# Kernel optimization log

Hardware: AMD Instinct MI355X
Metric: run time of the kernel (lower is better)

The kernel has to match this reference:

```python
import jax, jax.numpy as jnp
import numpy as np

A, NA, D_OBS, B = 16, 8, 64, 128  # agents, actions, obs dim, graphs
DZ = D_OBS + NA  # obs_z_input_dim = 72


def _mlp(x, W1, b1, W2, b2):
    # Linear -> leaky_relu(0.01) -> Linear, torch Linear convention (y = x @ W.T + b)
    return jax.nn.leaky_relu(x @ W1.T + b1) @ W2.T + b2


def setup_inputs() -> dict:
    key = jax.random.key(0)
    ks = iter(jax.random.split(key, 40))
    p = {}
    p["obs"] = jax.random.normal(next(ks), (B * A, D_OBS), jnp.float32)
    p["policies"] = jax.random.uniform(next(ks), (B * A, NA), jnp.float32)
    p["actions"] = jax.random.uniform(next(ks), (B * A, NA), jnp.float32)

    def mk(name, inp, out):
        p[name + "_w"] = jax.random.normal(next(ks), (out, inp), jnp.float32) / np.sqrt(inp).astype(np.float32)
        p[name + "_b"] = jax.random.normal(next(ks), (out,), jnp.float32) * 0.01

    mk("kw1", D_OBS, 64); mk("kw2", 64, 64)   # key_weight layers
    mk("qw1", D_OBS, 64); mk("qw2", 64, 64)   # query_weight layers
    mk("ko1", DZ, 64);    mk("ko2", 64, 64)   # key_obsz layers
    mk("qo1", DZ, 64);    mk("qo2", 64, 64)   # query_obsz layers
    mk("av1", DZ, 64);    mk("av2", 64, 64)   # attention_value_obsz layers
    mk("fv1", 128, 64);   mk("fv2", 64, 8)    # final_value layers
    return p


def reference(obs, policies, actions,
              kw1_w, kw1_b, kw2_w, kw2_b, qw1_w, qw1_b, qw2_w, qw2_b,
              ko1_w, ko1_b, ko2_w, ko2_b, qo1_w, qo1_b, qo2_w, qo2_b,
              av1_w, av1_b, av2_w, av2_b, fv1_w, fv1_b, fv2_w, fv2_b):
    d_k_w = jnp.sqrt(jnp.float32(kw2_w.shape[0]))
    d_k_o = jnp.sqrt(jnp.float32(ko2_w.shape[0]))
    Bn = obs.shape[0] // A
    obs_b = obs.reshape(Bn, A, -1)                      # [B,A,Dobs]
    pi = policies.reshape(Bn, A, NA)
    act = actions.reshape(Bn, A, NA)

    # --- DGL update_all on the fully-connected (with self-loop) per-batch graph ---
    key_z = _mlp(obs_b, kw1_w, kw1_b, kw2_w, kw2_b)     # [B,A,dk]
    query_z = _mlp(obs_b, qw1_w, qw1_b, qw2_w, qw2_b)
    score = jnp.einsum('bjd,bid->bij', key_z, query_z)  # src key j -> dst query i
    w = jax.nn.sigmoid(score / d_k_w)[..., None]        # [B,A,A,1], mailbox gate
    z = w * act[:, None] + (1.0 - w) * pi[:, None]      # [B,A(i),A(j),NA]
    weight_z = w.reshape(Bn * A, A, 1)

    # obs_z[b,i,j] = cat(obs[b,j], z[b,i,j])
    obs_rep = jnp.broadcast_to(obs_b[:, None], (Bn, A, A, obs_b.shape[-1]))
    obs_z = jnp.concatenate([obs_rep, z], axis=-1)      # [B,A,A,DZ]

    diag = jnp.arange(A)
    src = obs_z[:, diag, diag]                          # source_obs_z_: [B,A,DZ] (j==i entry)

    key_o = _mlp(src, ko1_w, ko1_b, ko2_w, ko2_b)       # broadcast over j
    query_o = _mlp(obs_z, qo1_w, qo1_b, qo2_w, qo2_b)   # [B,A,A,dk]
    score_o = jnp.einsum('bid,bijd->bij', key_o, query_o)
    weights_o = jax.nn.softmax(jnp.exp(jnp.clip(score_o / d_k_o, -5.0, 5.0)), axis=-1)  # [B,A,A]

    # obs_z_pi[b,i,j,k] = op[b,j] if k==j else obs_z[b,i,k], op = cat(obs, pi)
    op = jnp.concatenate([obs_b, pi], axis=-1)          # [B,A,DZ]
    m = jnp.eye(A, dtype=obs.dtype)[None, None, :, :, None]          # (j,k) mask
    obs_z_pi = obs_z[:, :, None] * (1.0 - m) + op[:, None, None] * m  # [B,A,A,A,DZ]

    attn_src = _mlp(src, av1_w, av1_b, av2_w, av2_b)                  # [B,A,O]
    attn_other = _mlp(obs_z_pi, av1_w, av1_b, av2_w, av2_b)           # [B,A,A,A,O]

    w_exp = weights_o[:, None, :, :, None]              # [b,i,j,k,1] = weights_o[b,j,k]
    mixed = jnp.mean(attn_other * w_exp, axis=-2)       # mean over k -> [B,A,A,O]
    src_rep = jnp.broadcast_to(attn_src[:, None], mixed.shape)
    node_features = jnp.concatenate([src_rep, mixed], axis=-1)        # [B,A,A,2O]
    value = _mlp(node_features, fv1_w, fv1_b, fv2_w, fv2_b)           # [B,A,A,8]

    weights_obsz = jnp.broadcast_to(w_exp, (Bn, A, A, A, 1))
    return value, weight_z, weights_obsz
```

## Files before the change

### kernel.cpp

```cpp
#include <hip/hip_runtime.h>

#define A_ 16
#define NA_ 8
#define DOBS_ 64

typedef _Float16 f16;
typedef f16 h2 __attribute__((ext_vector_type(2)));
typedef f16 v8h __attribute__((ext_vector_type(8)));
typedef float v4f __attribute__((ext_vector_type(4)));

__device__ __forceinline__ float fdot2f(h2 a, h2 b, float c) {
  return __builtin_amdgcn_fdot2(a, b, c, false);
}
__device__ __forceinline__ float lrelu(float x) { return x > 0.f ? x : 0.01f * x; }

struct P {
  const float *obs, *pol, *act;
  const float *kw1w, *kw1b, *kw2w, *kw2b, *qw1w, *qw1b, *qw2w, *qw2b;
  const float *ko1w, *ko1b, *ko2w, *ko2b, *qo1w, *qo1b, *qo2w, *qo2b;
  const float *av1w, *av1b, *av2w, *av2b, *fv1w, *fv1b, *fv2w, *fv2b;
  float *out0, *out1, *out2;
};

struct alignas(16) SM {
  f16 obsh[16 * 72];
  float pi[128];
  float act[128];
  float wsig[256];
  float wo[256];
  float c0[16];
  f16 eh[256];
  union {
    struct {
      f16 obsl[16 * 72];
      f16 Wp1[64 * 72], Wp2[64 * 72];
      f16 Wxh[64 * 72], Wxl[64 * 72];
      f16 X1h[16 * 72], X1l[16 * 72];
      f16 X2h[16 * 72], X2l[16 * 72];
      float S2[16 * 68];
      float S3G[16 * 68];
      float wz[512];
    } f;
    struct {
      f16 AOsrcD[16 * 72];
      f16 APT[64 * 24];
      f16 AextH[16 * 40];
      f16 fv2pw[512];
      f16 slice[8][1536];
      union { struct { f16 av1H[64 * 96]; f16 av2H[64 * 72]; } av; f16 fv1H[64 * 136]; } W;
      float av1b[64], av2b[64], fv1b[64], fv2b[8];
    } bk;
  } u;
};

__device__ __forceinline__ v4f gemm_plain(const f16* Xh, const f16* W, float bv, int nt, int lane) {
  const int m = lane & 15, q = lane >> 4;
  v4f acc = {bv, bv, bv, bv};
  const v8h a0 = *(const v8h*)(Xh + m * 72 + q * 8);
  const v8h a1 = *(const v8h*)(Xh + m * 72 + 32 + q * 8);
  const f16* wr = W + (nt * 16 + m) * 72 + q * 8;
  acc = __builtin_amdgcn_mfma_f32_16x16x32_f16(a0, *(const v8h*)wr, acc, 0, 0, 0);
  acc = __builtin_amdgcn_mfma_f32_16x16x32_f16(a1, *(const v8h*)(wr + 32), acc, 0, 0, 0);
  return acc;
}

__device__ __forceinline__ v4f gemm_tile(const f16* Xh, const f16* Xl,
                                         const f16* Wh, const f16* Wl,
                                         float bv, int nt, int lane) {
  const int m = lane & 15, q = lane >> 4;
  v4f acc = {bv, bv, bv, bv};
  const v8h ah0 = *(const v8h*)(Xh + m * 72 + q * 8);
  const v8h ah1 = *(const v8h*)(Xh + m * 72 + 32 + q * 8);
  const v8h al0 = *(const v8h*)(Xl + m * 72 + q * 8);
  const v8h al1 = *(const v8h*)(Xl + m * 72 + 32 + q * 8);
  const f16* wr = Wh + (nt * 16 + m) * 72 + q * 8;
  const v8h bh0 = *(const v8h*)(wr);
  const v8h bh1 = *(const v8h*)(wr + 32);
  const f16* wr2 = Wl + (nt * 16 + m) * 72 + q * 8;
  const v8h bl0 = *(const v8h*)(wr2);
  const v8h bl1 = *(const v8h*)(wr2 + 32);
  acc = __builtin_amdgcn_mfma_f32_16x16x32_f16(ah0, bh0, acc, 0, 0, 0);
  acc = __builtin_amdgcn_mfma_f32_16x16x32_f16(ah1, bh1, acc, 0, 0, 0);
  acc = __builtin_amdgcn_mfma_f32_16x16x32_f16(ah0, bl0, acc, 0, 0, 0);
  acc = __builtin_amdgcn_mfma_f32_16x16x32_f16(ah1, bl1, acc, 0, 0, 0);
  acc = __builtin_amdgcn_mfma_f32_16x16x32_f16(al0, bh0, acc, 0, 0, 0);
  acc = __builtin_amdgcn_mfma_f32_16x16x32_f16(al1, bh1, acc, 0, 0, 0);
  return acc;
}

__device__ __forceinline__ void writeX(f16* Xh, f16* Xl, v4f acc, int nt, int lane, bool relu) {
  const int m = lane & 15, q = lane >> 4;
#pragma unroll
  for (int reg = 0; reg < 4; reg++) {
    float y = acc[reg];
    if (relu) y = lrelu(y);
    const f16 yh = (f16)y;
    Xh[(q * 4 + reg) * 72 + nt * 16 + m] = yh;
    Xl[(q * 4 + reg) * 72 + nt * 16 + m] = (f16)(y - (float)yh);
  }
}

__device__ __forceinline__ void putP(f16* W, float4 v, int o, int rq) {
  h2* d = (h2*)(W + o * 72 + 4 * rq);
  d[0] = h2{(f16)v.x, (f16)v.y};
  d[1] = h2{(f16)v.z, (f16)v.w};
}

__device__ __forceinline__ void putW(f16* Wh, f16* Wl, float4 v, int o, int rq) {
  h2* dh = (h2*)(Wh + o * 72 + 4 * rq);
  h2* dl = (h2*)(Wl + o * 72 + 4 * rq);
  const f16 hx = (f16)v.x, hy = (f16)v.y, hz = (f16)v.z, hw = (f16)v.w;
  dh[0] = h2{hx, hy};
  dh[1] = h2{hz, hw};
  dl[0] = h2{(f16)(v.x - (float)hx), (f16)(v.y - (float)hy)};
  dl[1] = h2{(f16)(v.z - (float)hz), (f16)(v.w - (float)hw)};
}

__device__ __forceinline__ v8h bfrag(const f16* Wm, int stride, int nt, int ks, int lane) {
  const int n = lane & 15, q = lane >> 4;
  return *(const v8h*)(Wm + (nt * 16 + n) * stride + ks * 32 + q * 8);
}

__device__ __forceinline__ void av_mlp2(const f16* obsh, const f16* av1H, const f16* av2H,
                                        const float* av1b, const float* av2b,
                                        f16* Hbuf, v8h az, int lane, v4f acc2[4]) {
  const int m = lane & 15, q = lane >> 4;
  const v8h a0 = *(const v8h*)(obsh + m * 72 + q * 8);
  const v8h a1 = *(const v8h*)(obsh + m * 72 + 32 + q * 8);
#pragma unroll
  for (int nt = 0; nt < 4; nt++) {
    const float bv = av1b[nt * 16 + m];
    v4f acc = {bv, bv, bv, bv};
    acc = __builtin_amdgcn_mfma_f32_16x16x32_f16(a0, bfrag(av1H, 96, nt, 0, lane), acc, 0, 0, 0);
    acc = __builtin_amdgcn_mfma_f32_16x16x32_f16(a1, bfrag(av1H, 96, nt, 1, lane), acc, 0, 0, 0);
    acc = __builtin_amdgcn_mfma_f32_16x16x32_f16(az, bfrag(av1H, 96, nt, 2, lane), acc, 0, 0, 0);
#pragma unroll
    for (int reg = 0; reg < 4; reg++)
      Hbuf[(q * 4 + reg) * 72 + nt * 16 + m] = (f16)lrelu(acc[reg]);
  }
  const v8h h0 = *(const v8h*)(Hbuf + m * 72 + q * 8);
  const v8h h1 = *(const v8h*)(Hbuf + m * 72 + 32 + q * 8);
#pragma unroll
  for (int nt = 0; nt < 4; nt++) {
    const float bv = av2b[nt * 16 + m];
    v4f acc = {bv, bv, bv, bv};
    acc = __builtin_amdgcn_mfma_f32_16x16x32_f16(h0, bfrag(av2H, 72, nt, 0, lane), acc, 0, 0, 0);
    acc = __builtin_amdgcn_mfma_f32_16x16x32_f16(h1, bfrag(av2H, 72, nt, 1, lane), acc, 0, 0, 0);
    acc2[nt] = acc;
  }
}

__global__ __launch_bounds__(512) void critic_fused(P p) {
  __shared__ SM s;
  const int tid = threadIdx.x;
  const int b = blockIdx.x >> 1, ihalf = blockIdx.x & 1;
  const int w = tid >> 6, lane = tid & 63;
  const int m = lane & 15, quad = lane >> 4;
  const int o = tid & 63, r8 = tid >> 6;

  float4 Rkw1[2], Rkw2[2], Rqw1[2], Rqw2[2], Rko2[2], Rko1[2], Rqo1[2], Rqo2[2];
#pragma unroll
  for (int h = 0; h < 2; h++) {
    const int rq = r8 + 8 * h;
    Rkw1[h] = *(const float4*)(p.kw1w + o * 64 + 4 * rq);
    Rkw2[h] = *(const float4*)(p.kw2w + o * 64 + 4 * rq);
    Rqw1[h] = *(const float4*)(p.qw1w + o * 64 + 4 * rq);
    Rqw2[h] = *(const float4*)(p.qw2w + o * 64 + 4 * rq);
    Rko2[h] = *(const float4*)(p.ko2w + o * 64 + 4 * rq);
    Rko1[h] = *(const float4*)(p.ko1w + o * 72 + 4 * rq);
    Rqo1[h] = *(const float4*)(p.qo1w + o * 72 + 4 * rq);
    Rqo2[h].x = p.qo2w[(4 * rq + 0) * 64 + o];
    Rqo2[h].y = p.qo2w[(4 * rq + 1) * 64 + o];
    Rqo2[h].z = p.qo2w[(4 * rq + 2) * 64 + o];
    Rqo2[h].w = p.qo2w[(4 * rq + 3) * 64 + o];
  }
  const float Rwzko = p.ko1w[(tid >> 3) * 72 + 64 + (tid & 7)];
  const float Rwzqo = p.qo1w[(tid >> 3) * 72 + 64 + (tid & 7)];
  const int bi = (w & 3) * 16 + m;
  const float bias1 = (w < 4 ? p.kw1b : p.qw1b)[bi];
  const float bias2 = (w < 4 ? p.kw2b : p.qw2b)[bi];
  const float bias3 = (w < 4 ? p.ko1b : p.qo1b)[bi];
  const float bias4 = p.ko2b[bi];
  const float Bqo2_0 = p.qo2b[tid & 31];
  const float Bqo2_1 = p.qo2b[(tid & 31) + 32];
  const float4 rav1a = ((const float4*)p.av1w)[tid * 2];
  const float4 rav1b = ((const float4*)p.av1w)[tid * 2 + 1];
  const float rav1c = p.av1w[4096 + tid];
  const float4 rav2a = ((const float4*)p.av2w)[tid * 2];
  const float4 rav2b = ((const float4*)p.av2w)[tid * 2 + 1];
  float4 rfv[4];
#pragma unroll
  for (int qq = 0; qq < 4; qq++) rfv[qq] = ((const float4*)p.fv1w)[tid * 4 + qq];
  const float rfv2 = p.fv2w[tid];
  float rb1 = 0.f, rb2 = 0.f, rb3 = 0.f, rb4 = 0.f;
  if (tid < 64) { rb1 = p.av1b[tid]; rb2 = p.av2b[tid]; rb3 = p.fv1b[tid]; }
  if (tid < 8) rb4 = p.fv2b[tid];

  {
    const float2 ov = ((const float2*)(p.obs + (size_t)b * 1024))[tid];
    const int e0 = 2 * tid, r0 = e0 >> 6, c0i = e0 & 63;
    const f16 hx = (f16)ov.x, hy = (f16)ov.y;
    *(h2*)(s.obsh + r0 * 72 + c0i) = h2{hx, hy};
    *(h2*)(s.u.f.obsl + r0 * 72 + c0i) = h2{(f16)(ov.x - (float)hx), (f16)(ov.y - (float)hy)};
  }
  if (tid < 128) s.pi[tid] = p.pol[(size_t)b * 128 + tid];
  else if (tid < 256) s.act[tid - 128] = p.act[(size_t)b * 128 + tid - 128];
  s.u.f.wz[tid] = Rwzko;
  putP(s.u.f.Wp1, Rkw1[0], o, r8); putP(s.u.f.Wp1, Rkw1[1], o, r8 + 8);
  putP(s.u.f.Wp2, Rqw1[0], o, r8); putP(s.u.f.Wp2, Rqw1[1], o, r8 + 8);
  putW(s.u.f.Wxh, s.u.f.Wxl, Rko1[0], o, r8); putW(s.u.f.Wxh, s.u.f.Wxl, Rko1[1], o, r8 + 8);
  __syncthreads();

  {
    const f16* Wp = (w < 4) ? s.u.f.Wp1 : s.u.f.Wp2;
    f16* Xo = (w < 4) ? s.u.f.X1h : s.u.f.X2h;
    v4f a = gemm_plain(s.obsh, Wp, bias1, w & 3, lane);
#pragma unroll
    for (int reg = 0; reg < 4; reg++)
      Xo[(quad * 4 + reg) * 72 + (w & 3) * 16 + m] = (f16)lrelu(a[reg]);
  }
  __syncthreads();
  putP(s.u.f.Wp1, Rkw2[0], o, r8); putP(s.u.f.Wp1, Rkw2[1], o, r8 + 8);
  putP(s.u.f.Wp2, Rqw2[0], o, r8); putP(s.u.f.Wp2, Rqw2[1], o, r8 + 8);
  __syncthreads();

  {
    const f16* Wp = (w < 4) ? s.u.f.Wp1 : s.u.f.Wp2;
    const f16* Xi = (w < 4) ? s.u.f.X1h : s.u.f.X2h;
    float* So = (w < 4) ? s.u.f.S2 : s.u.f.S3G;
    v4f a = gemm_plain(Xi, Wp, bias2, w & 3, lane);
#pragma unroll
    for (int reg = 0; reg < 4; reg++)
      So[(quad * 4 + reg) * 68 + (w & 3) * 16 + m] = a[reg];
  }
  __syncthreads();

  {
    const int idx = tid >> 1, g2 = tid & 1;
    const int i = idx >> 4, j = idx & 15;
    float a0 = 0.f, a1 = 0.f, a2 = 0.f, a3 = 0.f;
#pragma unroll
    for (int t4 = 0; t4 < 8; t4++) {
      const float4 qv = *(const float4*)(s.u.f.S3G + i * 68 + g2 * 32 + 4 * t4);
      const float4 kv = *(const float4*)(s.u.f.S2 + j * 68 + g2 * 32 + 4 * t4);
      a0 += qv.x * kv.x; a1 += qv.y * kv.y; a2 += qv.z * kv.z; a3 += qv.w * kv.w;
    }
    float sc = (a0 + a1) + (a2 + a3);
    sc += __shfl_xor(sc, 1);
    if (g2 == 0) {
      const float wv = 1.f / (1.f + __expf(-sc * 0.125f));
      s.wsig[idx] = wv;
      p.out1[(size_t)b * 256 + idx] = wv;
    }
    putW(s.u.f.Wp1, s.u.f.Wp2, Rqo1[0], o, r8);
    putW(s.u.f.Wp1, s.u.f.Wp2, Rqo1[1], o, r8 + 8);
  }
  __syncthreads();

  if (w < 4) {
    v4f a = gemm_tile(s.obsh, s.u.f.obsl, s.u.f.Wxh, s.u.f.Wxl, bias3, w, lane);
    const int oo = w * 16 + m;
    float wzv[8];
    *(float4*)wzv = *(const float4*)(s.u.f.wz + oo * 8);
    *(float4*)(wzv + 4) = *(const float4*)(s.u.f.wz + oo * 8 + 4);
#pragma unroll
    for (int reg = 0; reg < 4; reg++) {
      const int rr = quad * 4 + reg;
      const float wrr = s.wsig[rr * 16 + rr];
      float zp = 0.f;
#pragma unroll
      for (int c = 0; c < 8; c++) {
        const float zc = s.pi[rr * 8 + c] + wrr * (s.act[rr * 8 + c] - s.pi[rr * 8 + c]);
        zp += wzv[c] * zc;
      }
      const float y = lrelu(a[reg] + zp);
      const f16 yh = (f16)y;
      s.u.f.X2h[rr * 72 + oo] = yh;
      s.u.f.X2l[rr * 72 + oo] = (f16)(y - (float)yh);
    }
  } else {
    v4f a = gemm_tile(s.obsh, s.u.f.obsl, s.u.f.Wp1, s.u.f.Wp2, bias3, w - 4, lane);
#pragma unroll
    for (int reg = 0; reg < 4; reg++)
      s.u.f.S3G[m * 68 + (quad * 4 + reg) * 4 + (w - 4)] = a[reg];
  }
  __syncthreads();

  putW(s.u.f.Wxh, s.u.f.Wxl, Rko2[0], o, r8); putW(s.u.f.Wxh, s.u.f.Wxl, Rko2[1], o, r8 + 8);
  putW(s.u.f.Wp1, s.u.f.Wp2, Rqo2[0], o, r8); putW(s.u.f.Wp1, s.u.f.Wp2, Rqo2[1], o, r8 + 8);
  { const int oo = tid >> 3, c = tid & 7; s.u.f.wz[(oo & 15) * 32 + (oo >> 4) * 8 + c] = Rwzqo; }
  __syncthreads();

  if (w < 4) {
    v4f a = gemm_tile(s.u.f.X2h, s.u.f.X2l, s.u.f.Wxh, s.u.f.Wxl, bias4, w, lane);
    writeX(s.u.f.X1h, s.u.f.X1l, a, w, lane, false);
  }
  __syncthreads();

  if (w < 4) {
    v4f a = gemm_tile(s.u.f.X1h, s.u.f.X1l, s.u.f.Wp1, s.u.f.Wp2, 0.f, w, lane);
#pragma unroll
    for (int reg = 0; reg < 4; reg++)
      s.u.f.S2[(quad * 4 + reg) * 68 + w * 16 + m] = a[reg];
  }
  {
    const int rr = tid >> 5, cc = tid & 31;
    const float kv0 = (float)s.u.f.X1h[rr * 72 + cc] + (float)s.u.f.X1l[rr * 72 + cc];
    const float kv1 = (float)s.u.f.X1h[rr * 72 + cc + 32] + (float)s.u.f.X1l[rr * 72 + cc + 32];
    float t = kv0 * Bqo2_0 + kv1 * Bqo2_1;
#pragma unroll
    for (int mk = 1; mk < 32; mk <<= 1) t += __shfl_xor(t, mk);
    if (cc == 0) s.c0[rr] = t;
  }
  __syncthreads();

  {
    const int idx = tid >> 1, g2 = tid & 1;
    const int i = idx >> 4, j = idx & 15;
    const float wij = s.wsig[i * 16 + j];
    float z[8];
#pragma unroll
    for (int c = 0; c < 8; c++) z[c] = s.pi[j * 8 + c] + wij * (s.act[j * 8 + c] - s.pi[j * 8 + c]);
    float sc = 0.f;
#pragma unroll
    for (int gg = 2 * g2; gg <= 2 * g2 + 1; gg++) {
#pragma unroll
      for (int t = 0; t < 16; t++) {
        const float4 wa = *(const float4*)(s.u.f.wz + t * 32 + gg * 8);
        const float4 wb = *(const float4*)(s.u.f.wz + t * 32 + gg * 8 + 4);
        float hv = s.u.f.S3G[t * 68 + j * 4 + gg]
          + wa.x * z[0] + wa.y * z[1] + wa.z * z[2] + wa.w * z[3]
          + wb.x * z[4] + wb.y * z[5] + wb.z * z[6] + wb.w * z[7];
        hv = lrelu(hv);
        sc += s.u.f.S2[i * 68 + gg * 16 + t] * hv;
      }
    }
    sc += __shfl_xor(sc, 1);
    if (g2 == 0) {
      float yv = (sc + s.c0[i]) * 0.125f;
      yv = fminf(fmaxf(yv, -5.f), 5.f);
      s.eh[idx] = (f16)__expf(yv);
    }
  }
  __syncthreads();

  if (tid < 256) {
    const int i = tid >> 4, j = tid & 15;
    float ev[16]; float mx = -1e30f;
#pragma unroll
    for (int jj = 0; jj < 16; jj++) { ev[jj] = (float)s.eh[i * 16 + jj]; mx = fmaxf(mx, ev[jj]); }
    float den = 0.f;
#pragma unroll
    for (int jj = 0; jj < 16; jj++) den += __expf(ev[jj] - mx);
    s.wo[tid] = __expf(ev[j] - mx) / den;
  }
  {
    float av1v[8] = {rav1a.x, rav1a.y, rav1a.z, rav1a.w, rav1b.x, rav1b.y, rav1b.z, rav1b.w};
#pragma unroll
    for (int e = 0; e < 8; e++) {
      const int k = tid * 8 + e, rr = k / 72, cc = k - rr * 72;
      s.u.bk.W.av.av1H[rr * 96 + cc] = (f16)av1v[e];
    }
    const int k = 4096 + tid, rr = k / 72, cc = k - rr * 72;
    s.u.bk.W.av.av1H[rr * 96 + cc] = (f16)rav1c;
    const int row = tid >> 3, c0p = 72 + (tid & 7) * 3;
#pragma unroll
    for (int c = 0; c < 3; c++) s.u.bk.W.av.av1H[row * 96 + c0p + c] = (f16)0.f;
    float av2v[8] = {rav2a.x, rav2a.y, rav2a.z, rav2a.w, rav2b.x, rav2b.y, rav2b.z, rav2b.w};
#pragma unroll
    for (int e = 0; e < 8; e++) {
      const int k2 = tid * 8 + e;
      s.u.bk.W.av.av2H[(k2 >> 6) * 72 + (k2 & 63)] = (f16)av2v[e];
    }
    s.u.bk.fv2pw[tid] = (f16)rfv2;
    if (tid < 64) { s.u.bk.av1b[tid] = rb1; s.u.bk.av2b[tid] = rb2; s.u.bk.fv1b[tid] = rb3; }
    if (tid < 8) s.u.bk.fv2b[tid] = rb4;
  }
  __syncthreads();

  {
    const int kk = tid >> 5, j2 = tid & 31;
    float v = 0.f;
    if (j2 < 16) v = s.wo[kk * 16 + j2] * 0.0625f;
    else if (j2 - 16 == kk) v = s.wo[kk * 16 + kk] * 0.0625f;
    s.u.bk.AextH[kk * 40 + j2] = (f16)v;
    const int q_ = tid >> 1, g2_ = tid & 1, k_ = q_ & 15;
    float* dst = p.out2 + ((size_t)b * 256 + q_) * 16 + 8 * g2_;
    *(float4*)(dst) = *(const float4*)(s.wo + k_ * 16 + 8 * g2_);
    *(float4*)(dst + 4) = *(const float4*)(s.wo + k_ * 16 + 8 * g2_ + 4);
  }
  __syncthreads();

  const int i_ = ihalf * 8 + w;
  f16* Sl = &s.u.bk.slice[w][0];
  {
    v8h az = {};
    if (quad == 0) {
      const float wv = s.wsig[i_ * 16 + m];
#pragma unroll
      for (int c = 0; c < 8; c++)
        az[c] = (f16)(s.pi[m * 8 + c] + wv * (s.act[m * 8 + c] - s.pi[m * 8 + c]));
    }
    v4f acc2[4];
    av_mlp2(s.obsh, s.u.bk.W.av.av1H, s.u.bk.W.av.av2H, s.u.bk.av1b, s.u.bk.av2b, Sl, az, lane, acc2);
#pragma unroll
    for (int nt = 0; nt < 4; nt++)
#pragma unroll
      for (int reg = 0; reg < 4; reg++)
        Sl[(nt * 16 + m) * 24 + quad * 4 + reg] = (f16)acc2[nt][reg];
  }
  if (w == 0) {
    v8h az = {};
    if (quad == 0) {
#pragma unroll
      for (int c = 0; c < 8; c++) az[c] = (f16)s.pi[m * 8 + c];
    }
    v4f acc2[4];
    av_mlp2(s.obsh, s.u.bk.W.av.av1H, s.u.bk.W.av.av2H, s.u.bk.av1b, s.u.bk.av2b, s.u.bk.APT, az, lane, acc2);
#pragma unroll
    for (int nt = 0; nt < 4; nt++)
#pragma unroll
      for (int reg = 0; reg < 4; reg++)
        s.u.bk.APT[(nt * 16 + m) * 24 + quad * 4 + reg] = (f16)acc2[nt][reg];
  }
  if (w == 1) {
    v8h az = {};
    if (quad == 0) {
      const float wv = s.wsig[m * 16 + m];
#pragma unroll
      for (int c = 0; c < 8; c++)
        az[c] = (f16)(s.pi[m * 8 + c] + wv * (s.act[m * 8 + c] - s.pi[m * 8 + c]));
    }
    v4f acc2[4];
    av_mlp2(s.obsh, s.u.bk.W.av.av1H, s.u.bk.W.av.av2H, s.u.bk.av1b, s.u.bk.av2b, s.u.bk.AOsrcD, az, lane, acc2);
#pragma unroll
    for (int nt = 0; nt < 4; nt++)
#pragma unroll
      for (int reg = 0; reg < 4; reg++)
        s.u.bk.AOsrcD[(quad * 4 + reg) * 72 + nt * 16 + m] = (f16)acc2[nt][reg];
  }
  __syncthreads();

#pragma unroll
  for (int qq = 0; qq < 4; qq++) {
    const int e0 = tid * 16 + qq * 4;
    h2* d = (h2*)&s.u.bk.W.fv1H[(e0 >> 7) * 136 + (e0 & 127)];
    d[0] = h2{(f16)rfv[qq].x, (f16)rfv[qq].y};
    d[1] = h2{(f16)rfv[qq].z, (f16)rfv[qq].w};
  }
  __syncthreads();

  {
    const v8h am = *(const v8h*)(&s.u.bk.AextH[m * 40 + quad * 8]);
    v4f macc[4];
#pragma unroll
    for (int nt = 0; nt < 4; nt++) {
      const int oo = nt * 16 + m;
      v8h bf;
      if (quad < 2) {
        bf = *(const v8h*)(Sl + oo * 24 + quad * 8);
      } else {
        const v8h apv = *(const v8h*)(&s.u.bk.APT[oo * 24 + (quad - 2) * 8]);
        const v8h aov = *(const v8h*)(Sl + oo * 24 + (quad - 2) * 8);
        bf = apv - aov;
      }
      v4f z4 = {0.f, 0.f, 0.f, 0.f};
      macc[nt] = __builtin_amdgcn_mfma_f32_16x16x32_f16(am, bf, z4, 0, 0, 0);
    }
#pragma unroll
    for (int nt = 0; nt < 4; nt++)
#pragma unroll
      for (int reg = 0; reg < 4; reg++)
        Sl[(quad * 4 + reg) * 72 + nt * 16 + m] = (f16)macc[nt][reg];
  }
  {
    const v8h f0 = *(const v8h*)(&s.u.bk.AOsrcD[m * 72 + quad * 8]);
    const v8h f1 = *(const v8h*)(&s.u.bk.AOsrcD[m * 72 + 32 + quad * 8]);
    const v8h f2 = *(const v8h*)(Sl + m * 72 + quad * 8);
    const v8h f3 = *(const v8h*)(Sl + m * 72 + 32 + quad * 8);
#pragma unroll
    for (int nt = 0; nt < 4; nt++) {
      const float bv = s.u.bk.fv1b[nt * 16 + m];
      v4f acc = {bv, bv, bv, bv};
      acc = __builtin_amdgcn_mfma_f32_16x16x32_f16(f0, bfrag(s.u.bk.W.fv1H, 136, nt, 0, lane), acc, 0, 0, 0);
      acc = __builtin_amdgcn_mfma_f32_16x16x32_f16(f1, bfrag(s.u.bk.W.fv1H, 136, nt, 1, lane), acc, 0, 0, 0);
      acc = __builtin_amdgcn_mfma_f32_16x16x32_f16(f2, bfrag(s.u.bk.W.fv1H, 136, nt, 2, lane), acc, 0, 0, 0);
      acc = __builtin_amdgcn_mfma_f32_16x16x32_f16(f3, bfrag(s.u.bk.W.fv1H, 136, nt, 3, lane), acc, 0, 0, 0);
#pragma unroll
      for (int reg = 0; reg < 4; reg++)
        Sl[(quad * 4 + reg) * 72 + nt * 16 + m] = (f16)lrelu(acc[reg]);
    }
  }
  {
    const int g2 = quad;
    float y0 = s.u.bk.fv2b[2 * g2], y1 = s.u.bk.fv2b[2 * g2 + 1];
#pragma unroll
    for (int o2 = 0; o2 < 32; o2++) {
      const h2 hh = *(const h2*)(Sl + m * 72 + 2 * o2);
      const h2 w0 = *(const h2*)(&s.u.bk.fv2pw[(2 * g2) * 64 + 2 * o2]);
      const h2 w1 = *(const h2*)(&s.u.bk.fv2pw[(2 * g2 + 1) * 64 + 2 * o2]);
      y0 = fdot2f(w0, hh, y0);
      y1 = fdot2f(w1, hh, y1);
    }
    *(float2*)(p.out0 + ((size_t)b * 256 + i_ * 16 + m) * 8 + 2 * g2) = make_float2(y0, y1);
  }
}

extern "C" void kernel_launch(void* const* d_in, const int* in_sizes, int n_in,
                              void* d_out, int out_size, void* d_ws, size_t ws_size,
                              hipStream_t stream) {
  P p;
  p.obs = (const float*)d_in[0];
  p.pol = (const float*)d_in[1];
  p.act = (const float*)d_in[2];
  p.kw1w = (const float*)d_in[3];  p.kw1b = (const float*)d_in[4];
  p.kw2w = (const float*)d_in[5];  p.kw2b = (const float*)d_in[6];
  p.qw1w = (const float*)d_in[7];  p.qw1b = (const float*)d_in[8];
  p.qw2w = (const float*)d_in[9];  p.qw2b = (const float*)d_in[10];
  p.ko1w = (const float*)d_in[11]; p.ko1b = (const float*)d_in[12];
  p.ko2w = (const float*)d_in[13]; p.ko2b = (const float*)d_in[14];
  p.qo1w = (const float*)d_in[15]; p.qo1b = (const float*)d_in[16];
  p.qo2w = (const float*)d_in[17]; p.qo2b = (const float*)d_in[18];
  p.av1w = (const float*)d_in[19]; p.av1b = (const float*)d_in[20];
  p.av2w = (const float*)d_in[21]; p.av2b = (const float*)d_in[22];
  p.fv1w = (const float*)d_in[23]; p.fv1b = (const float*)d_in[24];
  p.fv2w = (const float*)d_in[25]; p.fv2b = (const float*)d_in[26];

  const int Bn = in_sizes[0] / (A_ * DOBS_);
  p.out0 = (float*)d_out;
  p.out1 = p.out0 + (size_t)Bn * A_ * A_ * NA_;
  p.out2 = p.out1 + (size_t)Bn * A_ * A_;

  hipLaunchKernelGGL(critic_fused, dim3(2 * Bn), dim3(512), 0, stream, p);
}
```

Baseline: 127.6 us.

## Split each graph across four blocks and defer weight register loads

The grid now uses four blocks per graph instead of two. Each block handles four destination agents in the final stage, with waves 4 and 5 taking over the shared APT/AextH tasks, and the slice buffer shrinks to match. Weight loads into registers move from the kernel prologue to just before each stage uses them, and launch_bounds now requests 4 waves-per-EU, both meant to lower register pressure and raise occupancy. The trade-off is that the shared per-graph prologue (key/query MLPs, scores, attention values) is recomputed by twice as many blocks, and half the waves sit idle in the final stage.

```diff
diff --git a/kernel.cpp b/kernel.cpp
--- a/kernel.cpp
+++ b/kernel.cpp
@@ -46,7 +46,7 @@
       f16 APT[64 * 24];
       f16 AextH[16 * 40];
       f16 fv2pw[512];
-      f16 slice[8][1536];
+      f16 slice[4][1536];
       union { struct { f16 av1H[64 * 96]; f16 av2H[64 * 72]; } av; f16 fv1H[64 * 136]; } W;
       float av1b[64], av2b[64], fv1b[64], fv2b[8];
     } bk;
@@ -150,32 +150,28 @@
   }
 }
 
-__global__ __launch_bounds__(512) void critic_fused(P p) {
+__global__ __launch_bounds__(512, 4) void critic_fused(P p) {
   __shared__ SM s;
   const int tid = threadIdx.x;
-  const int b = blockIdx.x >> 1, ihalf = blockIdx.x & 1;
+  const int b = blockIdx.x >> 2, iq = blockIdx.x & 3;
   const int w = tid >> 6, lane = tid & 63;
   const int m = lane & 15, quad = lane >> 4;
   const int o = tid & 63, r8 = tid >> 6;
 
-  float4 Rkw1[2], Rkw2[2], Rqw1[2], Rqw2[2], Rko2[2], Rko1[2], Rqo1[2], Rqo2[2];
+  const float2 Robs = ((const float2*)(p.obs + (size_t)b * 1024))[tid];
+  float Rpa = 0.f;
+  if (tid < 128) Rpa = p.pol[(size_t)b * 128 + tid];
+  else if (tid < 256) Rpa = p.act[(size_t)b * 128 + tid - 128];
+  const float Rwzko = p.ko1w[(tid >> 3) * 72 + 64 + (tid & 7)];
+  const float Rwzqo = p.qo1w[(tid >> 3) * 72 + 64 + (tid & 7)];
+  float4 Rkw1[2], Rqw1[2], Rko1[2];
 #pragma unroll
   for (int h = 0; h < 2; h++) {
     const int rq = r8 + 8 * h;
     Rkw1[h] = *(const float4*)(p.kw1w + o * 64 + 4 * rq);
-    Rkw2[h] = *(const float4*)(p.kw2w + o * 64 + 4 * rq);
     Rqw1[h] = *(const float4*)(p.qw1w + o * 64 + 4 * rq);
-    Rqw2[h] = *(const float4*)(p.qw2w + o * 64 + 4 * rq);
-    Rko2[h] = *(const float4*)(p.ko2w + o * 64 + 4 * rq);
     Rko1[h] = *(const float4*)(p.ko1w + o * 72 + 4 * rq);
-    Rqo1[h] = *(const float4*)(p.qo1w + o * 72 + 4 * rq);
-    Rqo2[h].x = p.qo2w[(4 * rq + 0) * 64 + o];
-    Rqo2[h].y = p.qo2w[(4 * rq + 1) * 64 + o];
-    Rqo2[h].z = p.qo2w[(4 * rq + 2) * 64 + o];
-    Rqo2[h].w = p.qo2w[(4 * rq + 3) * 64 + o];
-  }
-  const float Rwzko = p.ko1w[(tid >> 3) * 72 + 64 + (tid & 7)];
-  const float Rwzqo = p.qo1w[(tid >> 3) * 72 + 64 + (tid & 7)];
+  }
   const int bi = (w & 3) * 16 + m;
   const float bias1 = (w < 4 ? p.kw1b : p.qw1b)[bi];
   const float bias2 = (w < 4 ? p.kw2b : p.qw2b)[bi];
@@ -183,34 +179,28 @@
   const float bias4 = p.ko2b[bi];
   const float Bqo2_0 = p.qo2b[tid & 31];
   const float Bqo2_1 = p.qo2b[(tid & 31) + 32];
-  const float4 rav1a = ((const float4*)p.av1w)[tid * 2];
-  const float4 rav1b = ((const float4*)p.av1w)[tid * 2 + 1];
-  const float rav1c = p.av1w[4096 + tid];
-  const float4 rav2a = ((const float4*)p.av2w)[tid * 2];
-  const float4 rav2b = ((const float4*)p.av2w)[tid * 2 + 1];
-  float4 rfv[4];
-#pragma unroll
-  for (int qq = 0; qq < 4; qq++) rfv[qq] = ((const float4*)p.fv1w)[tid * 4 + qq];
-  const float rfv2 = p.fv2w[tid];
-  float rb1 = 0.f, rb2 = 0.f, rb3 = 0.f, rb4 = 0.f;
-  if (tid < 64) { rb1 = p.av1b[tid]; rb2 = p.av2b[tid]; rb3 = p.fv1b[tid]; }
-  if (tid < 8) rb4 = p.fv2b[tid];
-
-  {
-    const float2 ov = ((const float2*)(p.obs + (size_t)b * 1024))[tid];
+
+  {
     const int e0 = 2 * tid, r0 = e0 >> 6, c0i = e0 & 63;
-    const f16 hx = (f16)ov.x, hy = (f16)ov.y;
+    const f16 hx = (f16)Robs.x, hy = (f16)Robs.y;
     *(h2*)(s.obsh + r0 * 72 + c0i) = h2{hx, hy};
-    *(h2*)(s.u.f.obsl + r0 * 72 + c0i) = h2{(f16)(ov.x - (float)hx), (f16)(ov.y - (float)hy)};
-  }
-  if (tid < 128) s.pi[tid] = p.pol[(size_t)b * 128 + tid];
-  else if (tid < 256) s.act[tid - 128] = p.act[(size_t)b * 128 + tid - 128];
+    *(h2*)(s.u.f.obsl + r0 * 72 + c0i) = h2{(f16)(Robs.x - (float)hx), (f16)(Robs.y - (float)hy)};
+  }
+  if (tid < 128) s.pi[tid] = Rpa;
+  else if (tid < 256) s.act[tid - 128] = Rpa;
   s.u.f.wz[tid] = Rwzko;
   putP(s.u.f.Wp1, Rkw1[0], o, r8); putP(s.u.f.Wp1, Rkw1[1], o, r8 + 8);
   putP(s.u.f.Wp2, Rqw1[0], o, r8); putP(s.u.f.Wp2, Rqw1[1], o, r8 + 8);
   putW(s.u.f.Wxh, s.u.f.Wxl, Rko1[0], o, r8); putW(s.u.f.Wxh, s.u.f.Wxl, Rko1[1], o, r8 + 8);
   __syncthreads();
 
+  float4 Rkw2[2], Rqw2[2];
+#pragma unroll
+  for (int h = 0; h < 2; h++) {
+    const int rq = r8 + 8 * h;
+    Rkw2[h] = *(const float4*)(p.kw2w + o * 64 + 4 * rq);
+    Rqw2[h] = *(const float4*)(p.qw2w + o * 64 + 4 * rq);
+  }
   {
     const f16* Wp = (w < 4) ? s.u.f.Wp1 : s.u.f.Wp2;
     f16* Xo = (w < 4) ? s.u.f.X1h : s.u.f.X2h;
@@ -224,6 +214,10 @@
   putP(s.u.f.Wp2, Rqw2[0], o, r8); putP(s.u.f.Wp2, Rqw2[1], o, r8 + 8);
   __syncthreads();
 
+  float4 Rqo1[2];
+#pragma unroll
+  for (int h = 0; h < 2; h++)
+    Rqo1[h] = *(const float4*)(p.qo1w + o * 72 + 4 * (r8 + 8 * h));
   {
     const f16* Wp = (w < 4) ? s.u.f.Wp1 : s.u.f.Wp2;
     const f16* Xi = (w < 4) ? s.u.f.X1h : s.u.f.X2h;
@@ -257,6 +251,16 @@
   }
   __syncthreads();
 
+  float4 Rko2[2], Rqo2[2];
+#pragma unroll
+  for (int h = 0; h < 2; h++) {
+    const int rq = r8 + 8 * h;
+    Rko2[h] = *(const float4*)(p.ko2w + o * 64 + 4 * rq);
+    Rqo2[h].x = p.qo2w[(4 * rq + 0) * 64 + o];
+    Rqo2[h].y = p.qo2w[(4 * rq + 1) * 64 + o];
+    Rqo2[h].z = p.qo2w[(4 * rq + 2) * 64 + o];
+    Rqo2[h].w = p.qo2w[(4 * rq + 3) * 64 + o];
+  }
   if (w < 4) {
     v4f a = gemm_tile(s.obsh, s.u.f.obsl, s.u.f.Wxh, s.u.f.Wxl, bias3, w, lane);
     const int oo = w * 16 + m;
@@ -314,6 +318,15 @@
   }
   __syncthreads();
 
+  const float4 rav1a = ((const float4*)p.av1w)[tid * 2];
+  const float4 rav1b = ((const float4*)p.av1w)[tid * 2 + 1];
+  const float rav1c = p.av1w[4096 + tid];
+  const float4 rav2a = ((const float4*)p.av2w)[tid * 2];
+  const float4 rav2b = ((const float4*)p.av2w)[tid * 2 + 1];
+  const float rfv2 = p.fv2w[tid];
+  float rb1 = 0.f, rb2 = 0.f, rb3 = 0.f, rb4 = 0.f;
+  if (tid < 64) { rb1 = p.av1b[tid]; rb2 = p.av2b[tid]; rb3 = p.fv1b[tid]; }
+  if (tid < 8) rb4 = p.fv2b[tid];
   {
     const int idx = tid >> 1, g2 = tid & 1;
     const int i = idx >> 4, j = idx & 15;
@@ -391,9 +404,12 @@
   }
   __syncthreads();
 
-  const int i_ = ihalf * 8 + w;
-  f16* Sl = &s.u.bk.slice[w][0];
-  {
+  float4 rfv[4];
+#pragma unroll
+  for (int qq = 0; qq < 4; qq++) rfv[qq] = ((const float4*)p.fv1w)[tid * 4 + qq];
+  const int i_ = iq * 4 + w;
+  f16* Sl = &s.u.bk.slice[w & 3][0];
+  if (w < 4) {
     v8h az = {};
     if (quad == 0) {
       const float wv = s.wsig[i_ * 16 + m];
@@ -409,7 +425,7 @@
       for (int reg = 0; reg < 4; reg++)
         Sl[(nt * 16 + m) * 24 + quad * 4 + reg] = (f16)acc2[nt][reg];
   }
-  if (w == 0) {
+  if (w == 4) {
     v8h az = {};
     if (quad == 0) {
 #pragma unroll
@@ -423,7 +439,7 @@
       for (int reg = 0; reg < 4; reg++)
         s.u.bk.APT[(nt * 16 + m) * 24 + quad * 4 + reg] = (f16)acc2[nt][reg];
   }
-  if (w == 1) {
+  if (w == 5) {
     v8h az = {};
     if (quad == 0) {
       const float wv = s.wsig[m * 16 + m];
@@ -450,59 +466,61 @@
   }
   __syncthreads();
 
-  {
-    const v8h am = *(const v8h*)(&s.u.bk.AextH[m * 40 + quad * 8]);
-    v4f macc[4];
-#pragma unroll
-    for (int nt = 0; nt < 4; nt++) {
-      const int oo = nt * 16 + m;
-      v8h bf;
-      if (quad < 2) {
-        bf = *(const v8h*)(Sl + oo * 24 + quad * 8);
-      } else {
-        const v8h apv = *(const v8h*)(&s.u.bk.APT[oo * 24 + (quad - 2) * 8]);
-        const v8h aov = *(const v8h*)(Sl + oo * 24 + (quad - 2) * 8);
-        bf = apv - aov;
+  if (w < 4) {
+    {
+      const v8h am = *(const v8h*)(&s.u.bk.AextH[m * 40 + quad * 8]);
+      v4f macc[4];
+#pragma unroll
+      for (int nt = 0; nt < 4; nt++) {
+        const int oo = nt * 16 + m;
+        v8h bf;
+        if (quad < 2) {
+          bf = *(const v8h*)(Sl + oo * 24 + quad * 8);
+        } else {
+          const v8h apv = *(const v8h*)(&s.u.bk.APT[oo * 24 + (quad - 2) * 8]);
+          const v8h aov = *(const v8h*)(Sl + oo * 24 + (quad - 2) * 8);
+          bf = apv - aov;
+        }
+        v4f z4 = {0.f, 0.f, 0.f, 0.f};
+        macc[nt] = __builtin_amdgcn_mfma_f32_16x16x32_f16(am, bf, z4, 0, 0, 0);
       }
-      v4f z4 = {0.f, 0.f, 0.f, 0.f};
-      macc[nt] = __builtin_amdgcn_mfma_f32_16x16x32_f16(am, bf, z4, 0, 0, 0);
-    }
-#pragma unroll
-    for (int nt = 0; nt < 4; nt++)
-#pragma unroll
-      for (int reg = 0; reg < 4; reg++)
-        Sl[(quad * 4 + reg) * 72 + nt * 16 + m] = (f16)macc[nt][reg];
-  }
-  {
-    const v8h f0 = *(const v8h*)(&s.u.bk.AOsrcD[m * 72 + quad * 8]);
-    const v8h f1 = *(const v8h*)(&s.u.bk.AOsrcD[m * 72 + 32 + quad * 8]);
-    const v8h f2 = *(const v8h*)(Sl + m * 72 + quad * 8);
-    const v8h f3 = *(const v8h*)(Sl + m * 72 + 32 + quad * 8);
-#pragma unroll
-    for (int nt = 0; nt < 4; nt++) {
-      const float bv = s.u.bk.fv1b[nt * 16 + m];
-      v4f acc = {bv, bv, bv, bv};
-      acc = __builtin_amdgcn_mfma_f32_16x16x32_f16(f0, bfrag(s.u.bk.W.fv1H, 136, nt, 0, lane), acc, 0, 0, 0);
-      acc = __builtin_amdgcn_mfma_f32_16x16x32_f16(f1, bfrag(s.u.bk.W.fv1H, 136, nt, 1, lane), acc, 0, 0, 0);
-      acc = __builtin_amdgcn_mfma_f32_16x16x32_f16(f2, bfrag(s.u.bk.W.fv1H, 136, nt, 2, lane), acc, 0, 0, 0);
-      acc = __builtin_amdgcn_mfma_f32_16x16x32_f16(f3, bfrag(s.u.bk.W.fv1H, 136, nt, 3, lane), acc, 0, 0, 0);
-#pragma unroll
-      for (int reg = 0; reg < 4; reg++)
-        Sl[(quad * 4 + reg) * 72 + nt * 16 + m] = (f16)lrelu(acc[reg]);
-    }
-  }
-  {
-    const int g2 = quad;
-    float y0 = s.u.bk.fv2b[2 * g2], y1 = s.u.bk.fv2b[2 * g2 + 1];
-#pragma unroll
-    for (int o2 = 0; o2 < 32; o2++) {
-      const h2 hh = *(const h2*)(Sl + m * 72 + 2 * o2);
-      const h2 w0 = *(const h2*)(&s.u.bk.fv2pw[(2 * g2) * 64 + 2 * o2]);
-      const h2 w1 = *(const h2*)(&s.u.bk.fv2pw[(2 * g2 + 1) * 64 + 2 * o2]);
-      y0 = fdot2f(w0, hh, y0);
-      y1 = fdot2f(w1, hh, y1);
-    }
-    *(float2*)(p.out0 + ((size_t)b * 256 + i_ * 16 + m) * 8 + 2 * g2) = make_float2(y0, y1);
+#pragma unroll
+      for (int nt = 0; nt < 4; nt++)
+#pragma unroll
+        for (int reg = 0; reg < 4; reg++)
+          Sl[(quad * 4 + reg) * 72 + nt * 16 + m] = (f16)macc[nt][reg];
+    }
+    {
+      const v8h f0 = *(const v8h*)(&s.u.bk.AOsrcD[m * 72 + quad * 8]);
+      const v8h f1 = *(const v8h*)(&s.u.bk.AOsrcD[m * 72 + 32 + quad * 8]);
+      const v8h f2 = *(const v8h*)(Sl + m * 72 + quad * 8);
+      const v8h f3 = *(const v8h*)(Sl + m * 72 + 32 + quad * 8);
+#pragma unroll
+      for (int nt = 0; nt < 4; nt++) {
+        const float bv = s.u.bk.fv1b[nt * 16 + m];
+        v4f acc = {bv, bv, bv, bv};
+        acc = __builtin_amdgcn_mfma_f32_16x16x32_f16(f0, bfrag(s.u.bk.W.fv1H, 136, nt, 0, lane), acc, 0, 0, 0);
+        acc = __builtin_amdgcn_mfma_f32_16x16x32_f16(f1, bfrag(s.u.bk.W.fv1H, 136, nt, 1, lane), acc, 0, 0, 0);
+        acc = __builtin_amdgcn_mfma_f32_16x16x32_f16(f2, bfrag(s.u.bk.W.fv1H, 136, nt, 2, lane), acc, 0, 0, 0);
+        acc = __builtin_amdgcn_mfma_f32_16x16x32_f16(f3, bfrag(s.u.bk.W.fv1H, 136, nt, 3, lane), acc, 0, 0, 0);
+#pragma unroll
+        for (int reg = 0; reg < 4; reg++)
+          Sl[(quad * 4 + reg) * 72 + nt * 16 + m] = (f16)lrelu(acc[reg]);
+      }
+    }
+    {
+      const int g2 = quad;
+      float y0 = s.u.bk.fv2b[2 * g2], y1 = s.u.bk.fv2b[2 * g2 + 1];
+#pragma unroll
+      for (int o2 = 0; o2 < 32; o2++) {
+        const h2 hh = *(const h2*)(Sl + m * 72 + 2 * o2);
+        const h2 w0 = *(const h2*)(&s.u.bk.fv2pw[(2 * g2) * 64 + 2 * o2]);
+        const h2 w1 = *(const h2*)(&s.u.bk.fv2pw[(2 * g2 + 1) * 64 + 2 * o2]);
+        y0 = fdot2f(w0, hh, y0);
+        y1 = fdot2f(w1, hh, y1);
+      }
+      *(float2*)(p.out0 + ((size_t)b * 256 + i_ * 16 + m) * 8 + 2 * g2) = make_float2(y0, y1);
+    }
   }
 }
 
@@ -531,5 +549,5 @@
   p.out1 = p.out0 + (size_t)Bn * A_ * A_ * NA_;
   p.out2 = p.out1 + (size_t)Bn * A_ * A_;
 
-  hipLaunchKernelGGL(critic_fused, dim3(2 * Bn), dim3(512), 0, stream, p);
-}
+  hipLaunchKernelGGL(critic_fused, dim3(4 * Bn), dim3(512), 0, stream, p);
+}
```

Result: slower. 139.1 us (+8.9%).
